# Performance work log

Measured on AMD Instinct MI355X. Metric: run time of the kernel, lower is better.

The kernel has to match this reference:

```python
import jax, jax.numpy as jnp
import numpy as np

B, D, H = 65536, 3, 256  # collocation batch, coord dim, hidden width


def setup_inputs() -> dict:
    key = jax.random.key(0)
    ks = jax.random.split(key, 8)

    def init(k, shape, fan_in):
        return jax.random.normal(k, shape, dtype=jnp.float32) * np.float32(1.0 / np.sqrt(fan_in))

    return {
        "x": jax.random.uniform(ks[0], (B, D), dtype=jnp.float32, minval=0.1, maxval=1.0),
        "W0": init(ks[1], (D, H), D), "b0": jnp.zeros((H,), jnp.float32),
        "W1": init(ks[2], (H, H), H), "b1": jnp.zeros((H,), jnp.float32),
        "W2": init(ks[3], (H, H), H), "b2": jnp.zeros((H,), jnp.float32),
        "W3": init(ks[4], (H, H), H), "b3": jnp.zeros((H,), jnp.float32),
        "Wout": init(ks[5], (H, 1), H), "bout": jnp.zeros((1,), jnp.float32),
    }


def reference(x, W0, b0, W1, b1, W2, b2, W3, b3, Wout, bout):
    # Scalar PINN network u(xi), xi: [D]
    def u_fn(xi):
        h = jnp.tanh(xi @ W0 + b0)
        h = jnp.tanh(h @ W1 + b1)
        h = jnp.tanh(h @ W2 + b2)
        h = jnp.tanh(h @ W3 + b3)
        return (h @ Wout + bout)[0]

    u = jax.vmap(u_fn)(x)                               # [B]
    # batch_gradient: du/dx_i for every coordinate axis (Cartesian: no adjustment)
    grads = jax.vmap(jax.grad(u_fn))(x)                 # [B, D]
    # batch_hessian diagonal: d^2u/dx_i^2 via forward-over-reverse
    hess_fn = jax.jacfwd(jax.grad(u_fn))                # [D, D] per sample
    hess_diag = jax.vmap(lambda xi: jnp.diagonal(hess_fn(xi)))(x)  # [B, D]
    # pack (u, grad, hessian-diagonal) as the PDE-residual ingredients
    return jnp.concatenate([u[:, None], grads, hess_diag], axis=1)  # [B, 1+D+D]
```

## Files before the change

### kernel.cpp

```cpp
#include <hip/hip_runtime.h>
#include <hip/hip_fp16.h>

#define HDIM 256
#define MS 16
#define LDAK 264
#define CSTRIDE (MS * LDAK * 2)

typedef _Float16 half8 __attribute__((ext_vector_type(8)));
typedef _Float16 half4 __attribute__((ext_vector_type(4)));
typedef _Float16 half2v __attribute__((ext_vector_type(2)));
typedef float f32x4 __attribute__((ext_vector_type(4)));

__device__ __forceinline__ float fast_tanh(float x) {
    float e = __expf(2.0f * x);
    return 1.0f - 2.0f * __builtin_amdgcn_rcpf(e + 1.0f);
}

__device__ __forceinline__ half4 cvt4(float a, float b, float c, float d) {
    half2v lo = __builtin_bit_cast(half2v, __builtin_amdgcn_cvt_pkrtz(a, b));
    half2v hi = __builtin_bit_cast(half2v, __builtin_amdgcn_cvt_pkrtz(c, d));
    half4 r; r[0] = lo[0]; r[1] = lo[1]; r[2] = hi[0]; r[3] = hi[1];
    return r;
}

__device__ __forceinline__ void barrier_lds() {
    asm volatile("s_waitcnt lgkmcnt(0)\n\ts_barrier" ::: "memory");
}

__global__ __launch_bounds__(256) void pack_weights(const float* __restrict__ W1,
                                                    const float* __restrict__ W2,
                                                    const float* __restrict__ W3,
                                                    _Float16* __restrict__ out) {
    int tid = blockIdx.x * 256 + threadIdx.x;
    int l = tid >> 13;
    int idx = tid & 8191;
    int kg = idx >> 8;
    int n = idx & 255;
    const float* W = (l == 0) ? W1 : (l == 1) ? W2 : W3;
    half8 v;
    #pragma unroll
    for (int j = 0; j < 8; ++j) v[j] = (_Float16)W[(kg * 8 + j) * 256 + n];
    *(half8*)(out + l * 65536 + kg * 2048 + n * 8) = v;
}

__global__ __launch_bounds__(512, 4)
void pinn_fused(const float* __restrict__ x,
                const float* __restrict__ W0,
                const float* __restrict__ b0,
                const float* __restrict__ b1,
                const float* __restrict__ b2,
                const float* __restrict__ b3,
                const float* __restrict__ Wout,
                const float* __restrict__ bout,
                const _Float16* __restrict__ Wp,
                float* __restrict__ out) {
    __shared__ __align__(16) _Float16 Abuf[7 * MS][LDAK];
    __shared__ float part[8 * 7 * MS];

    const int tid  = threadIdx.x;
    const int lane = tid & 63;
    const int wid  = tid >> 6;
    const int qd   = lane >> 4;
    const int n15  = lane & 15;
    const int base = blockIdx.x * MS;
    const int nw   = wid * 32 + n15;
    const int rot  = wid;

    const _Float16* Wbase = Wp + (qd * 256 + nw) * 8;

    const char* Ab = (const char*)Abuf;
    const int abase = (n15 * LDAK + qd * 8) * 2;
    char* Sb = (char*)Abuf;
    const int sbase = (n15 * LDAK + wid * 32 + qd * 4) * 2;

    half8 wf[2][2];

#define PREFJ(JJ) do { \
    if ((JJ) < 24) { \
        const int g_ = (((JJ) >> 3) * 8 + ((rot + ((JJ) & 7)) & 7)); \
        _Pragma("unroll") \
        for (int t_ = 0; t_ < 2; ++t_) \
            wf[(JJ) & 1][t_] = *(const half8*)(Wbase + g_ * 8192 + t_ * 128); \
    } \
} while (0)

#define LDAFS(AF, I) do { \
    const int so_ = ((rot + (I)) & 7) * 64; \
    _Pragma("unroll") \
    for (int c_ = 0; c_ < 7; ++c_) \
        AF[c_] = *(const half8*)(Ab + abase + c_ * CSTRIDE + so_); \
} while (0)

#define MMSJ(ACC, AF, JJ) do { \
    PREFJ((JJ) + 1); \
    __builtin_amdgcn_s_setprio(1); \
    _Pragma("unroll") \
    for (int c_ = 0; c_ < 7; ++c_) \
        _Pragma("unroll") \
        for (int t_ = 0; t_ < 2; ++t_) \
            ACC[c_][t_] = __builtin_amdgcn_mfma_f32_16x16x32_f16(wf[(JJ) & 1][t_], AF[c_], ACC[c_][t_], 0, 0, 0); \
    __builtin_amdgcn_s_setprio(0); \
} while (0)

#define KPRE(ACC, L) do { \
    half8 af_[7]; \
    LDAFS(af_, 0); \
    MMSJ(ACC, af_, (L) * 8 + 0); \
} while (0)

#define KPOST(ACC, L) do { \
    half8 af_[7]; \
    LDAFS(af_, 1); MMSJ(ACC, af_, (L) * 8 + 1); \
    LDAFS(af_, 2); MMSJ(ACC, af_, (L) * 8 + 2); \
    LDAFS(af_, 3); MMSJ(ACC, af_, (L) * 8 + 3); \
    LDAFS(af_, 4); MMSJ(ACC, af_, (L) * 8 + 4); \
    LDAFS(af_, 5); MMSJ(ACC, af_, (L) * 8 + 5); \
    LDAFS(af_, 6); MMSJ(ACC, af_, (L) * 8 + 6); \
    LDAFS(af_, 7); MMSJ(ACC, af_, (L) * 8 + 7); \
} while (0)

#define ZACC(A_) do { \
    _Pragma("unroll") \
    for (int c_ = 0; c_ < 7; ++c_) \
        _Pragma("unroll") \
        for (int t_ = 0; t_ < 2; ++t_) A_[c_][t_] = (f32x4){0.f, 0.f, 0.f, 0.f}; \
} while (0)

#define ELEMC(ACC, BB, EV) do { \
    _Pragma("unroll") \
    for (int tt_ = 0; tt_ < 2; ++tt_) { \
        const int ncol_ = wid * 32 + tt_ * 16 + qd * 4; \
        f32x4 bv_ = *(const f32x4*)((BB) + ncol_); \
        float tv_[4], gj_[3][4], sj_[3][4]; \
        _Pragma("unroll") \
        for (int r_ = 0; r_ < 4; ++r_) { \
            float zv_ = ACC[0][tt_][r_] + bv_[r_]; \
            tv_[r_] = fast_tanh(zv_); \
            float dd_ = 1.f - tv_[r_] * tv_[r_]; \
            float c2_ = -2.f * tv_[r_] * dd_; \
            _Pragma("unroll") \
            for (int i_ = 0; i_ < 3; ++i_) { \
                float zg_ = ACC[1 + i_][tt_][r_]; \
                float zs_ = ACC[4 + i_][tt_][r_]; \
                gj_[i_][r_] = dd_ * zg_; \
                sj_[i_][r_] = dd_ * zs_ + c2_ * zg_ * zg_; \
            } \
        } \
        EV[0][tt_] = cvt4(tv_[0], tv_[1], tv_[2], tv_[3]); \
        _Pragma("unroll") \
        for (int i_ = 0; i_ < 3; ++i_) { \
            EV[1 + i_][tt_] = cvt4(gj_[i_][0], gj_[i_][1], gj_[i_][2], gj_[i_][3]); \
            EV[4 + i_][tt_] = cvt4(sj_[i_][0], sj_[i_][1], sj_[i_][2], sj_[i_][3]); \
        } \
    } \
} while (0)

#define ELEMS(EV) do { \
    _Pragma("unroll") \
    for (int c_ = 0; c_ < 7; ++c_) \
        _Pragma("unroll") \
        for (int tt_ = 0; tt_ < 2; ++tt_) \
            *(half4*)(Sb + sbase + c_ * CSTRIDE + tt_ * 32) = EV[c_][tt_]; \
} while (0)

    f32x4 acc[7][2];
    half4 ev[7][2];

    ZACC(acc);
    PREFJ(0);

    {
        const int m  = tid & 15;
        const int n0 = (tid >> 4) * 8;
        const float x0 = x[(base + m) * 3 + 0];
        const float x1 = x[(base + m) * 3 + 1];
        const float x2 = x[(base + m) * 3 + 2];
        f32x4 w0v[2], w1v[2], w2v[2], bv[2];
        w0v[0] = *(const f32x4*)(W0 + n0);            w0v[1] = *(const f32x4*)(W0 + n0 + 4);
        w1v[0] = *(const f32x4*)(W0 + HDIM + n0);     w1v[1] = *(const f32x4*)(W0 + HDIM + n0 + 4);
        w2v[0] = *(const f32x4*)(W0 + 2 * HDIM + n0); w2v[1] = *(const f32x4*)(W0 + 2 * HDIM + n0 + 4);
        bv[0]  = *(const f32x4*)(b0 + n0);            bv[1]  = *(const f32x4*)(b0 + n0 + 4);
        half8 h[7];
        #pragma unroll
        for (int r = 0; r < 8; ++r) {
            const float w0 = w0v[r >> 2][r & 3];
            const float w1 = w1v[r >> 2][r & 3];
            const float w2 = w2v[r >> 2][r & 3];
            float z  = x0 * w0 + x1 * w1 + x2 * w2 + bv[r >> 2][r & 3];
            float tv = fast_tanh(z);
            float dd = 1.f - tv * tv;
            float c2 = -2.f * tv * dd;
            h[0][r] = (_Float16)tv;
            h[1][r] = (_Float16)(dd * w0);
            h[2][r] = (_Float16)(dd * w1);
            h[3][r] = (_Float16)(dd * w2);
            h[4][r] = (_Float16)(c2 * w0 * w0);
            h[5][r] = (_Float16)(c2 * w1 * w1);
            h[6][r] = (_Float16)(c2 * w2 * w2);
        }
        #pragma unroll
        for (int c = 0; c < 7; ++c)
            *(half8*)&Abuf[c * MS + m][n0] = h[c];
    }
    KPRE(acc, 0);
    barrier_lds();

    KPOST(acc, 0);
    ELEMC(acc, b1, ev);
    barrier_lds();
    ELEMS(ev);
    ZACC(acc);
    KPRE(acc, 1);
    barrier_lds();

    KPOST(acc, 1);
    ELEMC(acc, b2, ev);
    barrier_lds();
    ELEMS(ev);
    ZACC(acc);
    KPRE(acc, 2);
    barrier_lds();

    KPOST(acc, 2);
    {
        float p[7] = {0.f, 0.f, 0.f, 0.f, 0.f, 0.f, 0.f};
        #pragma unroll
        for (int t = 0; t < 2; ++t) {
            const int ncol = wid * 32 + t * 16 + qd * 4;
            f32x4 bv = *(const f32x4*)(b3 + ncol);
            f32x4 wv = *(const f32x4*)(Wout + ncol);
            #pragma unroll
            for (int r = 0; r < 4; ++r) {
                float zv = acc[0][t][r] + bv[r];
                float tv = fast_tanh(zv);
                float dd = 1.f - tv * tv;
                float c2 = -2.f * tv * dd;
                p[0] += tv * wv[r];
                #pragma unroll
                for (int i = 0; i < 3; ++i) {
                    float zg = acc[1 + i][t][r];
                    float zs = acc[4 + i][t][r];
                    p[1 + i] += (dd * zg) * wv[r];
                    p[4 + i] += (dd * zs + c2 * zg * zg) * wv[r];
                }
            }
        }
        #pragma unroll
        for (int c = 0; c < 7; ++c) {
            p[c] += __shfl_xor(p[c], 16, 64);
            p[c] += __shfl_xor(p[c], 32, 64);
        }
        if (lane < 16) {
            #pragma unroll
            for (int c = 0; c < 7; ++c)
                part[(wid * 7 + c) * MS + lane] = p[c];
        }
    }
    barrier_lds();

    if (tid < 7 * MS) {
        const int c = tid >> 4;
        const int m = tid & 15;
        float v = 0.f;
        #pragma unroll
        for (int w = 0; w < 8; ++w) v += part[(w * 7 + c) * MS + m];
        if (c == 0) v += bout[0];
        out[(base + m) * 7 + c] = v;
    }

#undef PREFJ
#undef LDAFS
#undef MMSJ
#undef KPRE
#undef KPOST
#undef ZACC
#undef ELEMC
#undef ELEMS
}

extern "C" void kernel_launch(void* const* d_in, const int* in_sizes, int n_in,
                              void* d_out, int out_size, void* d_ws, size_t ws_size,
                              hipStream_t stream) {
    const float* xp   = (const float*)d_in[0];
    const float* W0   = (const float*)d_in[1];
    const float* b0   = (const float*)d_in[2];
    const float* W1   = (const float*)d_in[3];
    const float* b1   = (const float*)d_in[4];
    const float* W2   = (const float*)d_in[5];
    const float* b2   = (const float*)d_in[6];
    const float* W3   = (const float*)d_in[7];
    const float* b3   = (const float*)d_in[8];
    const float* Wout = (const float*)d_in[9];
    const float* bout = (const float*)d_in[10];
    _Float16* Wp = (_Float16*)d_ws;

    pack_weights<<<96, 256, 0, stream>>>(W1, W2, W3, Wp);
    pinn_fused<<<65536 / MS, 512, 0, stream>>>(xp, W0, b0, b1, b2, b3, Wout, bout, Wp,
                                               (float*)d_out);
}
```

Measured before the change: 281.6 us.

## Drop weight prefetch double-buffer and register staging of activations

Replaces the double-buffered weight fragment prefetch with per-step loads inside a single KSTEP macro. The elementwise tanh/derivative stage now writes its fp16 results straight into LDS after the barrier, instead of holding them in registers across it. A barrier is also moved ahead of the first K step of layer 0. The aim is to cut VGPR pressure, possibly for occupancy or fewer spills. The cost is less overlap of global weight-load latency with MFMA work, and the lost early-start overlap around the barriers.

New measurement: 249.3 us. -11.5%, faster.

```diff
diff --git a/kernel.cpp b/kernel.cpp
--- a/kernel.cpp
+++ b/kernel.cpp
@@ -73,60 +73,40 @@
     char* Sb = (char*)Abuf;
     const int sbase = (n15 * LDAK + wid * 32 + qd * 4) * 2;
 
-    half8 wf[2][2];
-
-#define PREFJ(JJ) do { \
-    if ((JJ) < 24) { \
-        const int g_ = (((JJ) >> 3) * 8 + ((rot + ((JJ) & 7)) & 7)); \
+#define KSTEP(ACC, L, I) do { \
+    const int s_ = (rot + (I)) & 7; \
+    const int g_ = (L) * 8 + s_; \
+    half8 wf_[2]; \
+    wf_[0] = *(const half8*)(Wbase + g_ * 8192); \
+    wf_[1] = *(const half8*)(Wbase + g_ * 8192 + 128); \
+    half8 af_[7]; \
+    _Pragma("unroll") \
+    for (int c_ = 0; c_ < 7; ++c_) \
+        af_[c_] = *(const half8*)(Ab + abase + c_ * CSTRIDE + s_ * 64); \
+    __builtin_amdgcn_s_setprio(1); \
+    _Pragma("unroll") \
+    for (int c_ = 0; c_ < 7; ++c_) \
         _Pragma("unroll") \
         for (int t_ = 0; t_ < 2; ++t_) \
-            wf[(JJ) & 1][t_] = *(const half8*)(Wbase + g_ * 8192 + t_ * 128); \
-    } \
-} while (0)
-
-#define LDAFS(AF, I) do { \
-    const int so_ = ((rot + (I)) & 7) * 64; \
+            ACC[c_][t_] = __builtin_amdgcn_mfma_f32_16x16x32_f16(wf_[t_], af_[c_], ACC[c_][t_], 0, 0, 0); \
+    __builtin_amdgcn_s_setprio(0); \
+} while (0)
+
+#define KPRE(ACC, L) KSTEP(ACC, L, 0)
+
+#define KPOST(ACC, L) do { \
+    KSTEP(ACC, L, 1); KSTEP(ACC, L, 2); KSTEP(ACC, L, 3); KSTEP(ACC, L, 4); \
+    KSTEP(ACC, L, 5); KSTEP(ACC, L, 6); KSTEP(ACC, L, 7); \
+} while (0)
+
+#define ZACC(A_) do { \
     _Pragma("unroll") \
     for (int c_ = 0; c_ < 7; ++c_) \
-        AF[c_] = *(const half8*)(Ab + abase + c_ * CSTRIDE + so_); \
-} while (0)
-
-#define MMSJ(ACC, AF, JJ) do { \
-    PREFJ((JJ) + 1); \
-    __builtin_amdgcn_s_setprio(1); \
-    _Pragma("unroll") \
-    for (int c_ = 0; c_ < 7; ++c_) \
-        _Pragma("unroll") \
-        for (int t_ = 0; t_ < 2; ++t_) \
-            ACC[c_][t_] = __builtin_amdgcn_mfma_f32_16x16x32_f16(wf[(JJ) & 1][t_], AF[c_], ACC[c_][t_], 0, 0, 0); \
-    __builtin_amdgcn_s_setprio(0); \
-} while (0)
-
-#define KPRE(ACC, L) do { \
-    half8 af_[7]; \
-    LDAFS(af_, 0); \
-    MMSJ(ACC, af_, (L) * 8 + 0); \
-} while (0)
-
-#define KPOST(ACC, L) do { \
-    half8 af_[7]; \
-    LDAFS(af_, 1); MMSJ(ACC, af_, (L) * 8 + 1); \
-    LDAFS(af_, 2); MMSJ(ACC, af_, (L) * 8 + 2); \
-    LDAFS(af_, 3); MMSJ(ACC, af_, (L) * 8 + 3); \
-    LDAFS(af_, 4); MMSJ(ACC, af_, (L) * 8 + 4); \
-    LDAFS(af_, 5); MMSJ(ACC, af_, (L) * 8 + 5); \
-    LDAFS(af_, 6); MMSJ(ACC, af_, (L) * 8 + 6); \
-    LDAFS(af_, 7); MMSJ(ACC, af_, (L) * 8 + 7); \
-} while (0)
-
-#define ZACC(A_) do { \
-    _Pragma("unroll") \
-    for (int c_ = 0; c_ < 7; ++c_) \
         _Pragma("unroll") \
         for (int t_ = 0; t_ < 2; ++t_) A_[c_][t_] = (f32x4){0.f, 0.f, 0.f, 0.f}; \
 } while (0)
 
-#define ELEMC(ACC, BB, EV) do { \
+#define ELEM(ACC, BB) do { \
     _Pragma("unroll") \
     for (int tt_ = 0; tt_ < 2; ++tt_) { \
         const int ncol_ = wid * 32 + tt_ * 16 + qd * 4; \
@@ -146,28 +126,19 @@
                 sj_[i_][r_] = dd_ * zs_ + c2_ * zg_ * zg_; \
             } \
         } \
-        EV[0][tt_] = cvt4(tv_[0], tv_[1], tv_[2], tv_[3]); \
+        *(half4*)(Sb + sbase + 0 * CSTRIDE + tt_ * 32) = cvt4(tv_[0], tv_[1], tv_[2], tv_[3]); \
         _Pragma("unroll") \
         for (int i_ = 0; i_ < 3; ++i_) { \
-            EV[1 + i_][tt_] = cvt4(gj_[i_][0], gj_[i_][1], gj_[i_][2], gj_[i_][3]); \
-            EV[4 + i_][tt_] = cvt4(sj_[i_][0], sj_[i_][1], sj_[i_][2], sj_[i_][3]); \
+            *(half4*)(Sb + sbase + (1 + i_) * CSTRIDE + tt_ * 32) = \
+                cvt4(gj_[i_][0], gj_[i_][1], gj_[i_][2], gj_[i_][3]); \
+            *(half4*)(Sb + sbase + (4 + i_) * CSTRIDE + tt_ * 32) = \
+                cvt4(sj_[i_][0], sj_[i_][1], sj_[i_][2], sj_[i_][3]); \
         } \
     } \
 } while (0)
 
-#define ELEMS(EV) do { \
-    _Pragma("unroll") \
-    for (int c_ = 0; c_ < 7; ++c_) \
-        _Pragma("unroll") \
-        for (int tt_ = 0; tt_ < 2; ++tt_) \
-            *(half4*)(Sb + sbase + c_ * CSTRIDE + tt_ * 32) = EV[c_][tt_]; \
-} while (0)
-
     f32x4 acc[7][2];
-    half4 ev[7][2];
-
     ZACC(acc);
-    PREFJ(0);
 
     {
         const int m  = tid & 15;
@@ -202,21 +173,19 @@
         for (int c = 0; c < 7; ++c)
             *(half8*)&Abuf[c * MS + m][n0] = h[c];
     }
+    barrier_lds();
     KPRE(acc, 0);
-    barrier_lds();
 
     KPOST(acc, 0);
-    ELEMC(acc, b1, ev);
-    barrier_lds();
-    ELEMS(ev);
+    barrier_lds();
+    ELEM(acc, b1);
     ZACC(acc);
     KPRE(acc, 1);
     barrier_lds();
 
     KPOST(acc, 1);
-    ELEMC(acc, b2, ev);
-    barrier_lds();
-    ELEMS(ev);
+    barrier_lds();
+    ELEM(acc, b2);
     ZACC(acc);
     KPRE(acc, 2);
     barrier_lds();
@@ -268,14 +237,11 @@
         out[(base + m) * 7 + c] = v;
     }
 
-#undef PREFJ
-#undef LDAFS
-#undef MMSJ
+#undef KSTEP
 #undef KPRE
 #undef KPOST
 #undef ZACC
-#undef ELEMC
-#undef ELEMS
+#undef ELEM
 }
 
 extern "C" void kernel_launch(void* const* d_in, const int* in_sizes, int n_in,
```
